# Kernel optimization log

Hardware: AMD Instinct MI355X
Metric: run time of the kernel (lower is better)

Reference implementation:

```python
import jax, jax.numpy as jnp
import numpy as np

FEAT_STRIDE = 16
SCALES = np.array([8.0, 16.0, 32.0])
RATIOS = np.array([0.5, 1.0, 2.0])
A = 9  # anchors per location
PRE_NMS_TOPN = 6000   # TEST config (module in eval mode)
POST_NMS_TOPN = 300
NMS_THRESH = 0.7


def _generate_anchors(base_size=16):
    base = np.array([1.0, 1.0, base_size, base_size]) - 1.0  # [0,0,15,15]
    w = base[2] - base[0] + 1.0
    h = base[3] - base[1] + 1.0
    xc = base[0] + 0.5 * (w - 1.0)
    yc = base[1] + 0.5 * (h - 1.0)
    size = w * h
    ws = np.round(np.sqrt(size / RATIOS))
    hs = np.round(ws * RATIOS)
    ratio_anchors = np.stack([xc - 0.5 * (ws - 1), yc - 0.5 * (hs - 1),
                              xc + 0.5 * (ws - 1), yc + 0.5 * (hs - 1)], axis=1)
    out = []
    for ra in ratio_anchors:
        rw = ra[2] - ra[0] + 1.0
        rh = ra[3] - ra[1] + 1.0
        rxc = ra[0] + 0.5 * (rw - 1.0)
        ryc = ra[1] + 0.5 * (rh - 1.0)
        sw = rw * SCALES
        sh = rh * SCALES
        out.append(np.stack([rxc - 0.5 * (sw - 1), ryc - 0.5 * (sh - 1),
                             rxc + 0.5 * (sw - 1), ryc + 0.5 * (sh - 1)], axis=1))
    return np.concatenate(out, 0).astype(np.float32)  # [9,4]


def _all_anchors(H, W):
    a = _generate_anchors()
    sx = np.arange(W) * float(FEAT_STRIDE)
    sy = np.arange(H) * float(FEAT_STRIDE)
    sx, sy = np.meshgrid(sx, sy)
    shifts = np.stack([sx.ravel(), sy.ravel(), sx.ravel(), sy.ravel()], 1)  # [H*W,4]
    return (shifts[:, None, :] + a[None, :, :]).reshape(-1, 4).astype(np.float32)  # [H*W*A,4]


def _nms_sorted(boxes):
    # boxes: [N,4] already sorted by descending score; greedy NMS -> [POST_NMS_TOPN,4]
    x1, y1, x2, y2 = boxes[:, 0], boxes[:, 1], boxes[:, 2], boxes[:, 3]
    areas = (x2 - x1 + 1.0) * (y2 - y1 + 1.0)

    def body(i, st):
        valid, out_b = st
        idx = jnp.argmax(valid)          # first still-valid (highest score) box
        has = valid[idx]
        b = boxes[idx]
        xx1 = jnp.maximum(b[0], x1)
        yy1 = jnp.maximum(b[1], y1)
        xx2 = jnp.minimum(b[2], x2)
        yy2 = jnp.minimum(b[3], y2)
        inter = jnp.maximum(xx2 - xx1 + 1.0, 0.0) * jnp.maximum(yy2 - yy1 + 1.0, 0.0)
        iou = inter / (areas[idx] + areas - inter)
        valid = valid & (iou <= NMS_THRESH)  # suppresses idx itself (iou=1)
        out_b = out_b.at[i].set(jnp.where(has, b, jnp.zeros_like(b)))
        return valid, out_b

    valid0 = jnp.ones(boxes.shape[0], bool)
    out0 = jnp.zeros((POST_NMS_TOPN, 4), boxes.dtype)
    _, out_b = jax.lax.fori_loop(0, POST_NMS_TOPN, body, (valid0, out0))
    return out_b


def _rpn_forward(base_feat, im_info, W_conv, b_conv, W_cls, b_cls, W_bbox, b_bbox):
    B, C, H, W = base_feat.shape
    rpn_conv = jax.nn.relu(
        jax.lax.conv_general_dilated(base_feat, W_conv, (1, 1), 'SAME',
                                     dimension_numbers=('NCHW', 'OIHW', 'NCHW'))
        + b_conv[None, :, None, None])
    # 1x1 heads as channel matmuls
    cls_score = jnp.einsum('bchw,oc->bohw', rpn_conv, W_cls) + b_cls[None, :, None, None]
    bbox_pred = jnp.einsum('bchw,oc->bohw', rpn_conv, W_bbox) + b_bbox[None, :, None, None]
    # reshape(x,2) + softmax(dim=1) + reshape back == softmax over the (bg,fg) pair per anchor
    prob = jax.nn.softmax(cls_score.reshape(B, 2, A, H, W), axis=1)
    fg_scores = prob[:, 1].transpose(0, 2, 3, 1).reshape(B, -1)        # [B, H*W*A]
    deltas = bbox_pred.transpose(0, 2, 3, 1).reshape(B, -1, 4)         # [B, H*W*A, 4]

    anchors = jnp.asarray(_all_anchors(H, W))                          # [N,4]
    aw = anchors[:, 2] - anchors[:, 0] + 1.0
    ah = anchors[:, 3] - anchors[:, 1] + 1.0
    acx = anchors[:, 0] + 0.5 * aw
    acy = anchors[:, 1] + 0.5 * ah
    pcx = deltas[..., 0] * aw + acx
    pcy = deltas[..., 1] * ah + acy
    pw = jnp.exp(deltas[..., 2]) * aw
    ph = jnp.exp(deltas[..., 3]) * ah
    proposals = jnp.stack([pcx - 0.5 * pw, pcy - 0.5 * ph,
                           pcx + 0.5 * pw, pcy + 0.5 * ph], axis=-1)   # [B,N,4]
    imh = im_info[:, 0][:, None]
    imw = im_info[:, 1][:, None]
    proposals = jnp.stack([jnp.clip(proposals[..., 0], 0.0, imw - 1.0),
                           jnp.clip(proposals[..., 1], 0.0, imh - 1.0),
                           jnp.clip(proposals[..., 2], 0.0, imw - 1.0),
                           jnp.clip(proposals[..., 3], 0.0, imh - 1.0)], axis=-1)

    _, top_idx = jax.lax.top_k(fg_scores, PRE_NMS_TOPN)                # pre-NMS top-k
    top_boxes = jnp.take_along_axis(proposals, top_idx[..., None], axis=1)  # [B,K,4]
    kept = jax.vmap(_nms_sorted)(top_boxes)                            # [B,POST,4]
    batch_idx = jnp.broadcast_to(
        jnp.arange(B, dtype=kept.dtype)[:, None, None], (B, POST_NMS_TOPN, 1))
    rois = jnp.concatenate([batch_idx, kept], axis=-1)                 # [B,POST,5]
    return rois


def setup_inputs() -> dict:
    key = jax.random.key(0)
    ks = jax.random.split(key, 5)
    B, C, H, W = 4, 512, 64, 64
    base_feat = jax.random.normal(ks[0], (B, C, H, W), jnp.float32)
    im_info = jnp.tile(jnp.array([H * 16.0, W * 16.0, 1.0], jnp.float32), (B, 1))
    gt_boxes = jnp.zeros((B, 20, 5), jnp.float32)
    num_boxes = jnp.zeros((B,), jnp.int32)
    W_conv = jax.random.normal(ks[1], (512, C, 3, 3), jnp.float32) * 0.01
    b_conv = jnp.zeros((512,), jnp.float32)
    W_cls = jax.random.normal(ks[2], (2 * A, 512), jnp.float32) * 0.01
    b_cls = jnp.zeros((2 * A,), jnp.float32)
    W_bbox = jax.random.normal(ks[3], (4 * A, 512), jnp.float32) * 0.01
    b_bbox = jnp.zeros((4 * A,), jnp.float32)
    return {"base_feat": base_feat, "im_info": im_info, "gt_boxes": gt_boxes,
            "num_boxes": num_boxes, "W_conv": W_conv, "b_conv": b_conv,
            "W_cls": W_cls, "b_cls": b_cls, "W_bbox": W_bbox, "b_bbox": b_bbox}


def reference(base_feat, im_info, gt_boxes, num_boxes, W_conv, b_conv, W_cls, b_cls, W_bbox, b_bbox):
    # Eval-mode RPN: rois from ProposalLayer; rpn losses are 0 in eval.
    rois = _rpn_forward(base_feat, im_info, W_conv, b_conv, W_cls, b_cls, W_bbox, b_bbox)
    return rois
```

## Files before the change

### kernel.cpp

```cpp
#include <hip/hip_runtime.h>
#include <math.h>

constexpr int NB = 4;
constexpr int NC = 512;
constexpr int NH = 64, NW = 64;
constexpr int NPOS = NH * NW;
constexpr int NANCH = NPOS * 9;
constexpr int PRE_TOPN = 6000;
constexpr int POST_TOPN = 300;
constexpr int CAND_CAP = 40960;

typedef short short8_t __attribute__((ext_vector_type(8)));
typedef float f32x4_t __attribute__((ext_vector_type(4)));

__device__ __constant__ float A9c[9][4] = {
  {-84.f,-40.f,99.f,55.f},   {-176.f,-88.f,191.f,103.f}, {-360.f,-184.f,375.f,199.f},
  {-56.f,-56.f,71.f,71.f},   {-120.f,-120.f,135.f,135.f},{-248.f,-248.f,263.f,263.f},
  {-36.f,-80.f,51.f,95.f},   {-80.f,-168.f,95.f,183.f},  {-168.f,-344.f,183.f,359.f}};

constexpr size_t OFF_WB   = 0;
constexpr size_t OFF_IT   = 14155776;
constexpr size_t OFF_CONV = 47710208;
constexpr size_t OFF_HIST = 81264640;
constexpr size_t OFF_MISC = 81330176;
constexpr size_t OFF_HEAD = 0;
constexpr size_t OFF_SKEY = 3538944;
constexpr size_t OFF_BOX  = 4128768;
constexpr size_t OFF_CKEY = 6488064;
constexpr size_t OFF_CIDX = 7143424;
constexpr size_t OFF_SBOX = 7798784;

__device__ inline unsigned short f2bf(float f) {
  unsigned u = __float_as_uint(f);
  unsigned r = u + 0x7fffu + ((u >> 16) & 1u);
  return (unsigned short)(r >> 16);
}
__device__ inline float bf2f(unsigned short h) { return __uint_as_float(((unsigned)h) << 16); }

__device__ inline void split8(const float4 A, const float4 B, short8_t& h, short8_t& m, short8_t& l) {
#define SPL(J, X) { unsigned short hh = f2bf(X); float fh = bf2f(hh); \
                    unsigned short mm = f2bf((X) - fh); float fm = bf2f(mm); \
                    unsigned short ll = f2bf((X) - fh - fm); \
                    h[J] = (short)hh; m[J] = (short)mm; l[J] = (short)ll; }
  SPL(0, A.x) SPL(1, A.y) SPL(2, A.z) SPL(3, A.w)
  SPL(4, B.x) SPL(5, B.y) SPL(6, B.z) SPL(7, B.w)
#undef SPL
}

__global__ __launch_bounds__(256) void prep_k(const float* __restrict__ Wc,
                                              short* __restrict__ Wb,
                                              const float* __restrict__ in,
                                              float* __restrict__ It) {
  __shared__ float T[64][65];
  const int tid = threadIdx.x;
  if (blockIdx.x < 9216) {
    const int i = blockIdx.x * 256 + tid;
    const int tap = i >> 18;
    const int ko = (i >> 9) & 511, c = i & 511;
    const float w = Wc[(size_t)ko * 4608 + c * 9 + tap];
    const unsigned short h = f2bf(w);
    const float fh = bf2f(h);
    const unsigned short m = f2bf(w - fh);
    const float fm = bf2f(m);
    const unsigned short l = f2bf(w - fh - fm);
    const size_t base = ((size_t)tap * 3 * 512 + ko) * 512 + c;
    Wb[base] = (short)h;
    Wb[base + 512 * 512] = (short)m;
    Wb[base + 2 * 512 * 512] = (short)l;
  } else {
    const int id = blockIdx.x - 9216;
    const int pos0 = (id & 63) * 64;
    const int c0 = ((id >> 6) & 7) * 64;
    const int b = id >> 9;
    for (int i = tid; i < 4096; i += 256) {
      int cc = i >> 6, pp = i & 63;
      T[cc][pp] = in[(((size_t)b * 512 + c0 + cc) << 12) + pos0 + pp];
    }
    __syncthreads();
    for (int i = tid; i < 4096; i += 256) {
      int pp = i >> 6, cc = i & 63;
      It[((((size_t)b << 12) + pos0 + pp) << 9) + c0 + cc] = T[cc][pp];
    }
  }
}

__global__ __launch_bounds__(256, 2) void conv_mfma_k(
    const float* __restrict__ It, const short* __restrict__ Wb,
    const float* __restrict__ bias, float* __restrict__ out) {
  __shared__ short Slds[3 * 264 * 32];
  __shared__ short Wl[3 * 128 * 32];
  const int tid = threadIdx.x;
  const int wave = tid >> 6, lane = tid & 63;
  const int lm = lane & 15, lg = lane >> 4;
  const int pos0 = blockIdx.x * 128;
  const int ko0  = blockIdx.y * 128;
  const int b    = blockIdx.z;
  const int y0   = pos0 >> 6;

  f32x4_t acc[2][8];
  #pragma unroll
  for (int f = 0; f < 2; ++f)
    #pragma unroll
    for (int p = 0; p < 8; ++p) acc[f][p] = (f32x4_t){0.f, 0.f, 0.f, 0.f};

  short8_t pf[2][3];
#define PREF(TAP, C0S)                                                          \
  { _Pragma("unroll")                                                           \
    for (int t_ = 0; t_ < 2; ++t_) {                                            \
      const int i_ = tid + t_ * 256;                                            \
      const int kol_ = i_ >> 2, part_ = i_ & 3;                                 \
      const size_t g_ = (((size_t)(TAP) * 3) * 512 + ko0 + kol_) * 512 + (C0S) + (part_ << 3); \
      pf[t_][0] = *(const short8_t*)(Wb + g_);                                  \
      pf[t_][1] = *(const short8_t*)(Wb + g_ + 262144);                         \
      pf[t_][2] = *(const short8_t*)(Wb + g_ + 524288);                         \
    } }

  PREF(0, 0)

  for (int c0 = 0; c0 < 512; c0 += 32) {
    __syncthreads();
    for (int i = tid; i < 264; i += 256) {
      int r = i / 66, xx = i - r * 66;
      int gy = y0 + r - 1, gx = xx - 1;
      bool ok = ((unsigned)gy < 64u) && ((unsigned)gx < 64u);
      float4 f0 = {}, f1 = {}, f2 = {}, f3 = {}, f4 = {}, f5 = {}, f6 = {}, f7 = {};
      if (ok) {
        const float4* gp = (const float4*)(It + ((((size_t)b << 12) + (gy << 6) + gx) << 9) + c0);
        f0 = gp[0]; f1 = gp[1]; f2 = gp[2]; f3 = gp[3];
        f4 = gp[4]; f5 = gp[5]; f6 = gp[6]; f7 = gp[7];
      }
      const int sw = (xx >> 1) & 3;
      char* drow = (char*)Slds + (i << 6);
      short8_t h, m, l;
      split8(f0, f1, h, m, l);
      *(short8_t*)(drow + ((0 ^ sw) << 4)) = h;
      *(short8_t*)(drow + 16896 + ((0 ^ sw) << 4)) = m;
      *(short8_t*)(drow + 33792 + ((0 ^ sw) << 4)) = l;
      split8(f2, f3, h, m, l);
      *(short8_t*)(drow + ((1 ^ sw) << 4)) = h;
      *(short8_t*)(drow + 16896 + ((1 ^ sw) << 4)) = m;
      *(short8_t*)(drow + 33792 + ((1 ^ sw) << 4)) = l;
      split8(f4, f5, h, m, l);
      *(short8_t*)(drow + ((2 ^ sw) << 4)) = h;
      *(short8_t*)(drow + 16896 + ((2 ^ sw) << 4)) = m;
      *(short8_t*)(drow + 33792 + ((2 ^ sw) << 4)) = l;
      split8(f6, f7, h, m, l);
      *(short8_t*)(drow + ((3 ^ sw) << 4)) = h;
      *(short8_t*)(drow + 16896 + ((3 ^ sw) << 4)) = m;
      *(short8_t*)(drow + 33792 + ((3 ^ sw) << 4)) = l;
    }
    for (int tap = 0; tap < 9; ++tap) {
      __syncthreads();
      #pragma unroll
      for (int t_ = 0; t_ < 2; ++t_) {
        const int i_ = tid + t_ * 256;
        const int kol_ = i_ >> 2, part_ = i_ & 3;
        char* base = (char*)Wl + (kol_ << 6) + ((part_ ^ ((kol_ >> 1) & 3)) << 4);
        *(short8_t*)(base) = pf[t_][0];
        *(short8_t*)(base + 8192) = pf[t_][1];
        *(short8_t*)(base + 16384) = pf[t_][2];
      }
      __syncthreads();
      {
        const int ntap = (tap == 8) ? 0 : tap + 1;
        const int nc0  = (tap == 8) ? ((c0 + 32 < 512) ? c0 + 32 : c0) : c0;
        PREF(ntap, nc0)
      }
      const int dy = tap / 3, dx = tap - dy * 3;
      short8_t Ah[2], Am[2], Al[2];
      #pragma unroll
      for (int f = 0; f < 2; ++f) {
        int kol = (wave << 5) + (f << 4) + lm;
        char* ab = (char*)Wl + (kol << 6) + ((lg ^ ((kol >> 1) & 3)) << 4);
        Ah[f] = *(short8_t*)ab;
        Am[f] = *(short8_t*)(ab + 8192);
        Al[f] = *(short8_t*)(ab + 16384);
      }
      #pragma unroll
      for (int p = 0; p < 8; ++p) {
        const int yl = p >> 2;
        const int x  = ((p & 3) << 4) + lm;
        const int r  = yl + dy, xx = x + dx;
        char* bb = (char*)Slds + ((r * 66 + xx) << 6) + ((lg ^ ((xx >> 1) & 3)) << 4);
        short8_t Bh = *(short8_t*)bb;
        short8_t Bm = *(short8_t*)(bb + 16896);
        short8_t Bl = *(short8_t*)(bb + 33792);
        #pragma unroll
        for (int f = 0; f < 2; ++f) {
          acc[f][p] = __builtin_amdgcn_mfma_f32_16x16x32_bf16(Ah[f], Bh, acc[f][p], 0, 0, 0);
          acc[f][p] = __builtin_amdgcn_mfma_f32_16x16x32_bf16(Ah[f], Bm, acc[f][p], 0, 0, 0);
          acc[f][p] = __builtin_amdgcn_mfma_f32_16x16x32_bf16(Am[f], Bh, acc[f][p], 0, 0, 0);
          acc[f][p] = __builtin_amdgcn_mfma_f32_16x16x32_bf16(Ah[f], Bl, acc[f][p], 0, 0, 0);
          acc[f][p] = __builtin_amdgcn_mfma_f32_16x16x32_bf16(Al[f], Bh, acc[f][p], 0, 0, 0);
          acc[f][p] = __builtin_amdgcn_mfma_f32_16x16x32_bf16(Am[f], Bm, acc[f][p], 0, 0, 0);
        }
      }
    }
  }
#undef PREF
  #pragma unroll
  for (int f = 0; f < 2; ++f) {
    const int koB = ko0 + (wave << 5) + (f << 4) + (lg << 2);
    #pragma unroll
    for (int reg = 0; reg < 4; ++reg) {
      const float bv = bias[koB + reg];
      #pragma unroll
      for (int p = 0; p < 8; ++p) {
        const int pos = pos0 + (p << 4) + lm;
        out[(((size_t)b * 512 + koB + reg) << 12) + pos] = fmaxf(acc[f][p][reg] + bv, 0.f);
      }
    }
  }
}

__global__ __launch_bounds__(256, 4) void head_mfma_k(
    const float* __restrict__ conv, const float* __restrict__ Wcls,
    const float* __restrict__ bcls, const float* __restrict__ Wbbox,
    const float* __restrict__ bbbox, float* __restrict__ head) {
  __shared__ short Bl[3 * 64 * 32];
  __shared__ short Al[3 * 64 * 32];
  const int tid = threadIdx.x;
  const int wave = tid >> 6, lane = tid & 63;
  const int lm = lane & 15, lg = lane >> 4;
  const int pos0 = blockIdx.x * 64;
  const int b    = blockIdx.y;

  f32x4_t acc[4];
  #pragma unroll
  for (int f = 0; f < 4; ++f) acc[f] = (f32x4_t){0.f, 0.f, 0.f, 0.f};

  const float* cb = conv + ((size_t)b * 512 << 12);

  for (int c0 = 0; c0 < 512; c0 += 32) {
    __syncthreads();
    {
      const int pos_l = tid & 63, ch = tid >> 6;
      float v[8];
      #pragma unroll
      for (int j = 0; j < 8; ++j)
        v[j] = cb[((size_t)(c0 + ch * 8 + j) << 12) + pos0 + pos_l];
      short8_t h, m, l;
      split8(make_float4(v[0], v[1], v[2], v[3]), make_float4(v[4], v[5], v[6], v[7]), h, m, l);
      char* base = (char*)Bl + (pos_l << 6) + ((ch ^ ((pos_l >> 1) & 3)) << 4);
      *(short8_t*)(base) = h;
      *(short8_t*)(base + 4096) = m;
      *(short8_t*)(base + 8192) = l;
    }
    {
      const int ko = tid >> 2, part = tid & 3;
      float4 wa = {}, wb = {};
      if (ko < 54) {
        const float* src = (ko < 18) ? (Wcls + (size_t)ko * 512) : (Wbbox + (size_t)(ko - 18) * 512);
        wa = *(const float4*)(src + c0 + part * 8);
        wb = *(const float4*)(src + c0 + part * 8 + 4);
      }
      short8_t h, m, l;
      split8(wa, wb, h, m, l);
      char* base = (char*)Al + (ko << 6) + ((part ^ ((ko >> 1) & 3)) << 4);
      *(short8_t*)(base) = h;
      *(short8_t*)(base + 4096) = m;
      *(short8_t*)(base + 8192) = l;
    }
    __syncthreads();
    short8_t Bh, Bm, Bv;
    {
      const int pos_l = (wave << 4) + lm;
      char* bb = (char*)Bl + (pos_l << 6) + ((lg ^ ((pos_l >> 1) & 3)) << 4);
      Bh = *(short8_t*)bb;
      Bm = *(short8_t*)(bb + 4096);
      Bv = *(short8_t*)(bb + 8192);
    }
    #pragma unroll
    for (int f = 0; f < 4; ++f) {
      const int kol = (f << 4) + lm;
      char* ab = (char*)Al + (kol << 6) + ((lg ^ ((kol >> 1) & 3)) << 4);
      short8_t Ah = *(short8_t*)ab;
      short8_t Am = *(short8_t*)(ab + 4096);
      short8_t Av = *(short8_t*)(ab + 8192);
      acc[f] = __builtin_amdgcn_mfma_f32_16x16x32_bf16(Ah, Bh, acc[f], 0, 0, 0);
      acc[f] = __builtin_amdgcn_mfma_f32_16x16x32_bf16(Ah, Bm, acc[f], 0, 0, 0);
      acc[f] = __builtin_amdgcn_mfma_f32_16x16x32_bf16(Am, Bh, acc[f], 0, 0, 0);
      acc[f] = __builtin_amdgcn_mfma_f32_16x16x32_bf16(Ah, Bv, acc[f], 0, 0, 0);
      acc[f] = __builtin_amdgcn_mfma_f32_16x16x32_bf16(Av, Bh, acc[f], 0, 0, 0);
      acc[f] = __builtin_amdgcn_mfma_f32_16x16x32_bf16(Am, Bm, acc[f], 0, 0, 0);
    }
  }
  #pragma unroll
  for (int f = 0; f < 4; ++f) {
    #pragma unroll
    for (int reg = 0; reg < 4; ++reg) {
      const int ko = (f << 4) + (lg << 2) + reg;
      if (ko < 54) {
        const float bv = (ko < 18) ? bcls[ko] : bbbox[ko - 18];
        const int pos = pos0 + (wave << 4) + lm;
        head[(((size_t)b * 54 + ko) << 12) + pos] = acc[f][reg] + bv;
      }
    }
  }
}

__global__ __launch_bounds__(256) void decode_k(
    const float* __restrict__ head, const float* __restrict__ im_info,
    float* __restrict__ boxes, unsigned* __restrict__ skeys, unsigned* __restrict__ hist) {
  __shared__ unsigned hl[4096];
  const int tid = threadIdx.x;
  #pragma unroll
  for (int i = 0; i < 16; ++i) hl[tid + i * 256] = 0u;
  __syncthreads();
  const int p = blockIdx.x * 256 + tid;
  const int b = p >> 12; const int pos = p & 4095;
  const int x = pos & 63; const int y = pos >> 6;
  const float* hb = head + ((size_t)b * 54 << 12);
  const float imh = im_info[b * 3 + 0], imw = im_info[b * 3 + 1];
  float s[18];
  #pragma unroll
  for (int o = 0; o < 18; ++o) s[o] = hb[(o << 12) + pos];
  float d[36];
  #pragma unroll
  for (int o = 0; o < 36; ++o) d[o] = hb[((18 + o) << 12) + pos];
  const float sx = x * 16.f, sy = y * 16.f;
  #pragma unroll
  for (int a = 0; a < 9; ++a) {
    const float s0 = s[a], s1 = s[9 + a];
    const float m = fmaxf(s0, s1);
    const float e0 = expf(s0 - m), e1 = expf(s1 - m);
    const float score = e1 / (e0 + e1);
    const float d0 = d[a * 4 + 0], d1 = d[a * 4 + 1];
    const float d2 = d[a * 4 + 2], d3 = d[a * 4 + 3];
    const float ax1 = A9c[a][0] + sx, ay1 = A9c[a][1] + sy;
    const float ax2 = A9c[a][2] + sx, ay2 = A9c[a][3] + sy;
    const float aw = ax2 - ax1 + 1.f, ah = ay2 - ay1 + 1.f;
    const float acx = ax1 + 0.5f * aw, acy = ay1 + 0.5f * ah;
    const float pcx = d0 * aw + acx, pcy = d1 * ah + acy;
    const float pw = expf(d2) * aw, ph = expf(d3) * ah;
    const float x1 = fminf(fmaxf(pcx - 0.5f * pw, 0.f), imw - 1.f);
    const float y1 = fminf(fmaxf(pcy - 0.5f * ph, 0.f), imh - 1.f);
    const float x2 = fminf(fmaxf(pcx + 0.5f * pw, 0.f), imw - 1.f);
    const float y2 = fminf(fmaxf(pcy + 0.5f * ph, 0.f), imh - 1.f);
    const int n = pos * 9 + a;
    *(float4*)&boxes[((size_t)b * NANCH + n) * 4] = make_float4(x1, y1, x2, y2);
    const unsigned key = __float_as_uint(score);
    skeys[(size_t)b * NANCH + n] = key;
    atomicAdd(&hl[key >> 20], 1u);
  }
  __syncthreads();
  #pragma unroll
  for (int i = 0; i < 16; ++i) {
    unsigned c = hl[tid + i * 256];
    if (c) atomicAdd(&hist[b * 4096 + tid + i * 256], c);
  }
}

__global__ __launch_bounds__(512) void select_k(
    const unsigned* __restrict__ skeys, const unsigned* __restrict__ hist,
    unsigned* __restrict__ misc, unsigned* __restrict__ ckey,
    unsigned* __restrict__ cidx) {
  const int b = blockIdx.x;
  const int tid = threadIdx.x;
  __shared__ unsigned csum[256];
  __shared__ unsigned hl2[256];
  __shared__ unsigned s_t1, s_cumAbove, s_T2, s_cnt;
  const unsigned* h = hist + b * 4096;
  if (tid < 256) {
    unsigned s = 0;
    #pragma unroll
    for (int i = 0; i < 16; ++i) s += h[tid * 16 + i];
    csum[tid] = s;
    hl2[tid] = 0u;
  }
  __syncthreads();
  if (tid == 0) {
    unsigned cum = 0; int chunk = 0;
    for (int c = 255; c >= 0; --c) {
      if (cum + csum[c] >= (unsigned)PRE_TOPN) { chunk = c; break; }
      cum += csum[c];
    }
    unsigned t1 = chunk * 16, cumAbove = cum;
    for (int i = 15; i >= 0; --i) {
      unsigned cnt = h[chunk * 16 + i];
      if (cum + cnt >= (unsigned)PRE_TOPN) { t1 = chunk * 16 + i; cumAbove = cum; break; }
      cum += cnt;
    }
    s_t1 = t1; s_cumAbove = cumAbove; s_cnt = 0u;
  }
  __syncthreads();
  const unsigned t1 = s_t1;
  const unsigned* sk = skeys + (size_t)b * NANCH;
  for (int t = tid; t < NANCH; t += 512) {
    unsigned key = sk[t];
    if ((key >> 20) == t1) atomicAdd(&hl2[(key >> 12) & 255u], 1u);
  }
  __syncthreads();
  if (tid == 0) {
    unsigned cum = s_cumAbove;
    unsigned T2 = t1 << 20;
    for (int ss = 255; ss >= 0; --ss) {
      unsigned c = hl2[ss];
      if (cum + c >= (unsigned)PRE_TOPN) { T2 = (t1 << 20) | ((unsigned)ss << 12); break; }
      cum += c;
    }
    s_T2 = T2;
  }
  __syncthreads();
  const unsigned T2 = s_T2;
  const int lane = tid & 63;
  for (int t = tid; t < NANCH; t += 512) {
    unsigned key = sk[t];
    bool pred = key >= T2;
    unsigned long long mb = __ballot(pred);
    unsigned base = 0;
    if (lane == 0) base = atomicAdd(&s_cnt, (unsigned)__popcll(mb));
    base = (unsigned)__shfl((int)base, 0, 64);
    if (pred) {
      unsigned pp = base + (unsigned)__popcll(mb & ((1ull << lane) - 1ull));
      if (pp < (unsigned)CAND_CAP) {
        ckey[(size_t)b * CAND_CAP + pp] = key;
        cidx[(size_t)b * CAND_CAP + pp] = (unsigned)t;
      }
    }
  }
  __syncthreads();
  if (tid == 0) misc[12 + b] = s_cnt;
}

__global__ __launch_bounds__(256) void rank_scatter_k(
    const unsigned* __restrict__ ckey, const unsigned* __restrict__ cidx,
    const unsigned* __restrict__ misc, const float* __restrict__ boxes,
    float* __restrict__ sbox) {
  const int b = blockIdx.y;
  const int K = min((int)misc[12 + b], CAND_CAP);
  if (blockIdx.x * 256 >= (unsigned)K) return;
  const int i = blockIdx.x * 256 + threadIdx.x;
  unsigned mykey = 0, myidx = 0;
  const bool active = i < K;
  if (active) {
    mykey = ckey[(size_t)b * CAND_CAP + i];
    myidx = cidx[(size_t)b * CAND_CAP + i];
  }
  int rank = 0;
  __shared__ unsigned skey[1024];
  __shared__ unsigned sidx[1024];
  for (int c0 = 0; c0 < K; c0 += 1024) {
    int n = min(1024, K - c0);
    __syncthreads();
    for (int e = threadIdx.x; e < n; e += 256) {
      skey[e] = ckey[(size_t)b * CAND_CAP + c0 + e];
      sidx[e] = cidx[(size_t)b * CAND_CAP + c0 + e];
    }
    __syncthreads();
    if (active) {
      for (int j = 0; j < n; ++j) {
        unsigned kj = skey[j];
        rank += (kj > mykey) || (kj == mykey && sidx[j] < myidx);
      }
    }
  }
  if (active && rank < PRE_TOPN) {
    float4 bx = *(const float4*)&boxes[((size_t)b * NANCH + myidx) * 4];
    *(float4*)&sbox[((size_t)b * PRE_TOPN + rank) * 4] = bx;
  }
}

__global__ __launch_bounds__(256) void nms_fused_k(const float* __restrict__ sbox,
                                                   float* __restrict__ out) {
  __shared__ float4 tb[64];
  __shared__ float4 pk[POST_TOPN];
  __shared__ unsigned long long supw[4];
  __shared__ int s_np;
  const int b = blockIdx.x;
  const int tid = threadIdx.x;
  const int wv = tid >> 6, lane = tid & 63;
  const float* S = sbox + (size_t)b * PRE_TOPN * 4;
  float* O = out + (size_t)b * POST_TOPN * 5;
  if (tid == 0) s_np = 0;
  int np = 0;

  for (int t = 0; t < (PRE_TOPN + 63) / 64; ++t) {
    __syncthreads();
    np = s_np;
    if (np >= POST_TOPN) break;
    const int nt = min(64, PRE_TOPN - t * 64);
    if (tid < 64 && tid < nt) tb[tid] = *(const float4*)&S[(size_t)(t * 64 + tid) * 4];
    __syncthreads();
    const float4 q = tb[lane < nt ? lane : 0];
    const float qarea = (q.z - q.x + 1.f) * (q.w - q.y + 1.f);
    bool sup = false;
    for (int p = wv; p < np; p += 4) {
      const float4 pb = pk[p];
      const float pa = (pb.z - pb.x + 1.f) * (pb.w - pb.y + 1.f);
      const float xx1 = fmaxf(pb.x, q.x), yy1 = fmaxf(pb.y, q.y);
      const float xx2 = fminf(pb.z, q.z), yy2 = fminf(pb.w, q.w);
      const float inter = fmaxf(xx2 - xx1 + 1.f, 0.f) * fmaxf(yy2 - yy1 + 1.f, 0.f);
      const float iou = inter / (pa + qarea - inter);
      sup = sup || (iou > 0.7f);
    }
    unsigned long long bal = __ballot(sup);
    if (lane == 0) supw[wv] = bal;
    __syncthreads();
    if (wv == 0) {
      const unsigned long long validm = (nt == 64) ? ~0ull : ((1ull << nt) - 1ull);
      unsigned long long remaining = validm & ~(supw[0] | supw[1] | supw[2] | supw[3]);
      while (remaining && np < POST_TOPN) {
        const int jj = __ffsll((long long)remaining) - 1;
        const float4 pb = tb[jj];
        if (lane == 0) {
          pk[np] = pb;
          O[np * 5 + 0] = (float)b;
          O[np * 5 + 1] = pb.x; O[np * 5 + 2] = pb.y;
          O[np * 5 + 3] = pb.z; O[np * 5 + 4] = pb.w;
        }
        const float pa = (pb.z - pb.x + 1.f) * (pb.w - pb.y + 1.f);
        const float xx1 = fmaxf(pb.x, q.x), yy1 = fmaxf(pb.y, q.y);
        const float xx2 = fminf(pb.z, q.z), yy2 = fminf(pb.w, q.w);
        const float inter = fmaxf(xx2 - xx1 + 1.f, 0.f) * fmaxf(yy2 - yy1 + 1.f, 0.f);
        const float iou = inter / (pa + qarea - inter);
        remaining &= ~__ballot(iou > 0.7f);
        ++np;
      }
      if (lane == 0) s_np = np;
    }
  }
  __syncthreads();
  np = s_np;
  for (int e = tid; e < (POST_TOPN - np) * 5; e += 256) {
    int r = np + e / 5; int c = e - (e / 5) * 5;
    O[r * 5 + c] = (c == 0) ? (float)b : 0.f;
  }
}

extern "C" void kernel_launch(void* const* d_in, const int* in_sizes, int n_in,
                              void* d_out, int out_size, void* d_ws, size_t ws_size,
                              hipStream_t stream) {
  const float* base_feat = (const float*)d_in[0];
  const float* im_info   = (const float*)d_in[1];
  const float* W_conv    = (const float*)d_in[4];
  const float* b_conv    = (const float*)d_in[5];
  const float* W_cls     = (const float*)d_in[6];
  const float* b_cls     = (const float*)d_in[7];
  const float* W_bbox    = (const float*)d_in[8];
  const float* b_bbox    = (const float*)d_in[9];
  float* out = (float*)d_out;
  char* ws = (char*)d_ws;

  short*    Wb    = (short*)(ws + OFF_WB);
  float*    It    = (float*)(ws + OFF_IT);
  float*    conv  = (float*)(ws + OFF_CONV);
  float*    head  = (float*)(ws + OFF_HEAD);
  unsigned* skeys = (unsigned*)(ws + OFF_SKEY);
  float*    boxes = (float*)(ws + OFF_BOX);
  unsigned* hist  = (unsigned*)(ws + OFF_HIST);
  unsigned* misc  = (unsigned*)(ws + OFF_MISC);
  unsigned* ckey  = (unsigned*)(ws + OFF_CKEY);
  unsigned* cidx  = (unsigned*)(ws + OFF_CIDX);
  float*    sbox  = (float*)(ws + OFF_SBOX);

  hipMemsetAsync(ws + OFF_HIST, 0, 65536 + 256, stream);

  prep_k<<<9216 + 2048, 256, 0, stream>>>(W_conv, Wb, base_feat, It);
  conv_mfma_k<<<dim3(32, 4, 4), 256, 0, stream>>>(It, Wb, b_conv, conv);
  head_mfma_k<<<dim3(64, 4), 256, 0, stream>>>(conv, W_cls, b_cls, W_bbox, b_bbox, head);
  decode_k<<<64, 256, 0, stream>>>(head, im_info, boxes, skeys, hist);
  select_k<<<4, 512, 0, stream>>>(skeys, hist, misc, ckey, cidx);
  rank_scatter_k<<<dim3(CAND_CAP / 256, 4), 256, 0, stream>>>(ckey, cidx, misc, boxes, sbox);
  nms_fused_k<<<4, 256, 0, stream>>>(sbox, out);
}
```

Measured before the change: 730.5 us.

## Load conv weight fragments directly into registers, dropping the LDS staging buffer

The weight (A) operand of the 3x9-plane split-bf16 conv MFMA is now loaded by each wave straight from global memory into register fragments, using a double-buffered A0/A1 register prefetch. This removes the per-tap LDS weight store and the two __syncthreads per tap. The freed LDS and the launch bound raised from 2 to 3 blocks per SM are meant to allow higher occupancy. In exchange, global weight loads are no longer shared across waves and are narrower per row, more registers are needed, and the tap loop is fully unrolled.

Result: slower. 1.383 ms (+89.3%).

```diff
diff --git a/kernel.cpp b/kernel.cpp
--- a/kernel.cpp
+++ b/kernel.cpp
@@ -84,11 +84,10 @@
   }
 }
 
-__global__ __launch_bounds__(256, 2) void conv_mfma_k(
+__global__ __launch_bounds__(256, 3) void conv_mfma_k(
     const float* __restrict__ It, const short* __restrict__ Wb,
     const float* __restrict__ bias, float* __restrict__ out) {
   __shared__ short Slds[3 * 264 * 32];
-  __shared__ short Wl[3 * 128 * 32];
   const int tid = threadIdx.x;
   const int wave = tid >> 6, lane = tid & 63;
   const int lm = lane & 15, lg = lane >> 4;
@@ -103,19 +102,38 @@
     #pragma unroll
     for (int p = 0; p < 8; ++p) acc[f][p] = (f32x4_t){0.f, 0.f, 0.f, 0.f};
 
-  short8_t pf[2][3];
-#define PREF(TAP, C0S)                                                          \
+  short8_t A0[2][3], A1[2][3];
+#define LOADA(DST, TAP, C0S)                                                    \
   { _Pragma("unroll")                                                           \
-    for (int t_ = 0; t_ < 2; ++t_) {                                            \
-      const int i_ = tid + t_ * 256;                                            \
-      const int kol_ = i_ >> 2, part_ = i_ & 3;                                 \
-      const size_t g_ = (((size_t)(TAP) * 3) * 512 + ko0 + kol_) * 512 + (C0S) + (part_ << 3); \
-      pf[t_][0] = *(const short8_t*)(Wb + g_);                                  \
-      pf[t_][1] = *(const short8_t*)(Wb + g_ + 262144);                         \
-      pf[t_][2] = *(const short8_t*)(Wb + g_ + 524288);                         \
+    for (int f_ = 0; f_ < 2; ++f_) {                                            \
+      const int koRow_ = ko0 + (wave << 5) + (f_ << 4) + lm;                    \
+      _Pragma("unroll")                                                         \
+      for (int pl_ = 0; pl_ < 3; ++pl_)                                         \
+        DST[f_][pl_] = *(const short8_t*)(Wb +                                  \
+          (((size_t)((TAP) * 3 + pl_) * 512 + koRow_) << 9) + (C0S) + (lg << 3)); \
     } }
 
-  PREF(0, 0)
+#define TAPMFMA(AARR)                                                           \
+  { _Pragma("unroll")                                                           \
+    for (int p_ = 0; p_ < 8; ++p_) {                                            \
+      const int yl_ = p_ >> 2;                                                  \
+      const int x_  = ((p_ & 3) << 4) + lm;                                     \
+      const int r_  = yl_ + dy, xx_ = x_ + dx;                                  \
+      char* bb_ = (char*)Slds + ((r_ * 66 + xx_) << 6) + ((lg ^ ((xx_ >> 1) & 3)) << 4); \
+      short8_t Bh_ = *(short8_t*)bb_;                                           \
+      short8_t Bm_ = *(short8_t*)(bb_ + 16896);                                 \
+      short8_t Bl_ = *(short8_t*)(bb_ + 33792);                                 \
+      _Pragma("unroll")                                                         \
+      for (int f_ = 0; f_ < 2; ++f_) {                                          \
+        acc[f_][p_] = __builtin_amdgcn_mfma_f32_16x16x32_bf16(AARR[f_][0], Bh_, acc[f_][p_], 0, 0, 0); \
+        acc[f_][p_] = __builtin_amdgcn_mfma_f32_16x16x32_bf16(AARR[f_][0], Bm_, acc[f_][p_], 0, 0, 0); \
+        acc[f_][p_] = __builtin_amdgcn_mfma_f32_16x16x32_bf16(AARR[f_][1], Bh_, acc[f_][p_], 0, 0, 0); \
+        acc[f_][p_] = __builtin_amdgcn_mfma_f32_16x16x32_bf16(AARR[f_][0], Bl_, acc[f_][p_], 0, 0, 0); \
+        acc[f_][p_] = __builtin_amdgcn_mfma_f32_16x16x32_bf16(AARR[f_][2], Bh_, acc[f_][p_], 0, 0, 0); \
+        acc[f_][p_] = __builtin_amdgcn_mfma_f32_16x16x32_bf16(AARR[f_][1], Bm_, acc[f_][p_], 0, 0, 0); \
+      } } }
+
+  LOADA(A0, 0, 0)
 
   for (int c0 = 0; c0 < 512; c0 += 32) {
     __syncthreads();
@@ -149,55 +167,27 @@
       *(short8_t*)(drow + 16896 + ((3 ^ sw) << 4)) = m;
       *(short8_t*)(drow + 33792 + ((3 ^ sw) << 4)) = l;
     }
+    __syncthreads();
+    #pragma unroll
     for (int tap = 0; tap < 9; ++tap) {
-      __syncthreads();
-      #pragma unroll
-      for (int t_ = 0; t_ < 2; ++t_) {
-        const int i_ = tid + t_ * 256;
-        const int kol_ = i_ >> 2, part_ = i_ & 3;
-        char* base = (char*)Wl + (kol_ << 6) + ((part_ ^ ((kol_ >> 1) & 3)) << 4);
-        *(short8_t*)(base) = pf[t_][0];
-        *(short8_t*)(base + 8192) = pf[t_][1];
-        *(short8_t*)(base + 16384) = pf[t_][2];
-      }
-      __syncthreads();
+      const int dy = tap / 3, dx = tap - dy * 3;
       {
         const int ntap = (tap == 8) ? 0 : tap + 1;
         const int nc0  = (tap == 8) ? ((c0 + 32 < 512) ? c0 + 32 : c0) : c0;
-        PREF(ntap, nc0)
-      }
-      const int dy = tap / 3, dx = tap - dy * 3;
-      short8_t Ah[2], Am[2], Al[2];
+        if (tap & 1) { LOADA(A0, ntap, nc0) }
+        else         { LOADA(A1, ntap, nc0) }
+      }
+      if (tap & 1) { TAPMFMA(A1) }
+      else         { TAPMFMA(A0) }
+    }
+    #pragma unroll
+    for (int f = 0; f < 2; ++f)
       #pragma unroll
-      for (int f = 0; f < 2; ++f) {
-        int kol = (wave << 5) + (f << 4) + lm;
-        char* ab = (char*)Wl + (kol << 6) + ((lg ^ ((kol >> 1) & 3)) << 4);
-        Ah[f] = *(short8_t*)ab;
-        Am[f] = *(short8_t*)(ab + 8192);
-        Al[f] = *(short8_t*)(ab + 16384);
-      }
-      #pragma unroll
-      for (int p = 0; p < 8; ++p) {
-        const int yl = p >> 2;
-        const int x  = ((p & 3) << 4) + lm;
-        const int r  = yl + dy, xx = x + dx;
-        char* bb = (char*)Slds + ((r * 66 + xx) << 6) + ((lg ^ ((xx >> 1) & 3)) << 4);
-        short8_t Bh = *(short8_t*)bb;
-        short8_t Bm = *(short8_t*)(bb + 16896);
-        short8_t Bl = *(short8_t*)(bb + 33792);
-        #pragma unroll
-        for (int f = 0; f < 2; ++f) {
-          acc[f][p] = __builtin_amdgcn_mfma_f32_16x16x32_bf16(Ah[f], Bh, acc[f][p], 0, 0, 0);
-          acc[f][p] = __builtin_amdgcn_mfma_f32_16x16x32_bf16(Ah[f], Bm, acc[f][p], 0, 0, 0);
-          acc[f][p] = __builtin_amdgcn_mfma_f32_16x16x32_bf16(Am[f], Bh, acc[f][p], 0, 0, 0);
-          acc[f][p] = __builtin_amdgcn_mfma_f32_16x16x32_bf16(Ah[f], Bl, acc[f][p], 0, 0, 0);
-          acc[f][p] = __builtin_amdgcn_mfma_f32_16x16x32_bf16(Al[f], Bh, acc[f][p], 0, 0, 0);
-          acc[f][p] = __builtin_amdgcn_mfma_f32_16x16x32_bf16(Am[f], Bm, acc[f][p], 0, 0, 0);
-        }
-      }
-    }
-  }
-#undef PREF
+      for (int pl = 0; pl < 3; ++pl)
+        A0[f][pl] = A1[f][pl];
+  }
+#undef LOADA
+#undef TAPMFMA
   #pragma unroll
   for (int f = 0; f < 2; ++f) {
     const int koB = ko0 + (wave << 5) + (f << 4) + (lg << 2);
```
